# Kernel optimization log

Measured on AMD Instinct MI355X. Metric: run time of the kernel, lower is better.

The kernel has to match this reference:

```python
import jax, jax.numpy as jnp
import numpy as np

LN_EPS = 1e-5

def _layernorm(x, w, b):
    mu = jnp.mean(x, axis=-1, keepdims=True)
    var = jnp.mean(jnp.square(x - mu), axis=-1, keepdims=True)
    return (x - mu) * jax.lax.rsqrt(var + LN_EPS) * w + b

def setup_inputs() -> dict:
    key = jax.random.key(0)
    ks = jax.random.split(key, 6)
    B, NQ, QD = 8, 576, 4096
    NKV, KVD = 2304, 1024
    s = 0.02
    return {
        "x_q": jax.random.normal(ks[0], (B, NQ, QD), jnp.float32),
        "x_kv": jax.random.normal(ks[1], (B, NKV, KVD), jnp.float32),
        "q_ln_w": jnp.ones((QD,), jnp.float32),
        "q_ln_b": jnp.zeros((QD,), jnp.float32),
        "q_w": jax.random.normal(ks[2], (QD, QD), jnp.float32) * s,
        "q_b": jnp.zeros((QD,), jnp.float32),
        "k_ln_w": jnp.ones((KVD,), jnp.float32),
        "k_ln_b": jnp.zeros((KVD,), jnp.float32),
        "k_w": jax.random.normal(ks[3], (KVD, QD), jnp.float32) * s,
        "k_b": jnp.zeros((QD,), jnp.float32),
        "v_ln_w": jnp.ones((KVD,), jnp.float32),
        "v_ln_b": jnp.zeros((KVD,), jnp.float32),
        "v_w": jax.random.normal(ks[4], (KVD, QD), jnp.float32) * s,
        "v_b": jnp.zeros((QD,), jnp.float32),
    }

def reference(x_q, x_kv, q_ln_w, q_ln_b, q_w, q_b,
              k_ln_w, k_ln_b, k_w, k_b, v_ln_w, v_ln_b, v_w, v_b):
    B, NQ, QD = x_q.shape
    hw = int(round(x_kv.shape[1] ** 0.5))          # 48
    KVD = x_kv.shape[-1]
    patch_num = int(round(NQ ** 0.5))              # 24
    patch_size = hw // patch_num                   # 2
    # 'b (h w) d -> b h w d' then group into patch_num x patch_num windows
    kv = x_kv.reshape(B, hw, hw, KVD)
    kv = kv.reshape(B, patch_num, patch_size, patch_num, patch_size, KVD)
    kv = kv.transpose(0, 1, 3, 2, 4, 5).reshape(B, patch_num * patch_num, patch_size * patch_size, KVD)
    # projections (LayerNorm + Linear)
    q = _layernorm(x_q, q_ln_w, q_ln_b) @ q_w + q_b            # [B, P2, QD]
    k = _layernorm(kv, k_ln_w, k_ln_b) @ k_w + k_b             # [B, P2, S2, QD]
    v = _layernorm(kv, v_ln_w, v_ln_b) @ v_w + v_b             # [B, P2, S2, QD]
    scale = 1.0 / (QD ** 0.5)
    att = jnp.einsum('bpd,bpsd->bps', q, k) * scale            # [B, P2, S2]
    att = jnp.nan_to_num(att)
    att = jax.nn.softmax(att, axis=-1)
    feat = jnp.einsum('bps,bpsd->bpd', att, v)                 # [B, P2, QD]
    return (x_q, feat)
```

## Files before the change

kernel.cpp:

```cpp
#include <hip/hip_runtime.h>
#include <cstdint>
#include <cstddef>


typedef __attribute__((ext_vector_type(8))) short short8;
typedef __attribute__((ext_vector_type(4))) float f32x4;

#define DEV __device__ __forceinline__

DEV unsigned short f2bf(float f) {
  union { float f; unsigned u; } x; x.f = f;
  unsigned r = x.u + 0x7fffu + ((x.u >> 16) & 1u);
  return (unsigned short)(r >> 16);
}
DEV float bf2f(unsigned short u) {
  union { unsigned u; float f; } x; x.u = ((unsigned)u) << 16;
  return x.f;
}

DEV void gload16(const void* g, void* l) {
  __builtin_amdgcn_global_load_lds(
      (const __attribute__((address_space(1))) unsigned int*)g,
      (__attribute__((address_space(3))) unsigned int*)l, 16, 0, 0);
}

template <bool OUT_BF16, bool HAS_BIAS>
__global__ __launch_bounds__(256, 2) void gemm_nt(
    const unsigned short* __restrict__ A, const unsigned short* __restrict__ Bm,
    void* __restrict__ Cv, const float* __restrict__ bias, int M, int N, int K) {
  __shared__ __align__(16) unsigned short lds_a[128 * 32];
  __shared__ __align__(16) unsigned short lds_b[128 * 32];
  const int t = threadIdx.x;
  const int l = t & 63;
  const int w = t >> 6;
  const long brow = (long)blockIdx.x * 128;
  const long bcol = (long)blockIdx.y * 128;

  const int srow = t >> 2;
  const int scol = (t & 3) * 8;
  const unsigned short* a0 = A + (brow + srow) * (long)K + scol;
  const unsigned short* a1 = A + (brow + 64 + srow) * (long)K + scol;
  const unsigned short* b0 = Bm + (bcol + srow) * (long)K + scol;
  const unsigned short* b1 = Bm + (bcol + 64 + srow) * (long)K + scol;
  unsigned short* la0 = lds_a + t * 8;
  unsigned short* la1 = lds_a + 2048 + t * 8;
  unsigned short* lb0 = lds_b + t * 8;
  unsigned short* lb1 = lds_b + 2048 + t * 8;

  const int wr = w >> 1, wc = w & 1;
  const int fr = l & 15;
  const int fk = (l >> 4) * 8;

  f32x4 acc[4][4] = {};

  for (int kt = 0; kt < K; kt += 32) {
    __syncthreads();
    gload16(a0 + kt, la0);
    gload16(a1 + kt, la1);
    gload16(b0 + kt, lb0);
    gload16(b1 + kt, lb1);
    asm volatile("s_waitcnt vmcnt(0)" ::: "memory");
    __syncthreads();
    short8 af[4], bf[4];
#pragma unroll
    for (int mi = 0; mi < 4; ++mi)
      af[mi] = *(const short8*)&lds_a[(wr * 64 + mi * 16 + fr) * 32 + fk];
#pragma unroll
    for (int ni = 0; ni < 4; ++ni)
      bf[ni] = *(const short8*)&lds_b[(wc * 64 + ni * 16 + fr) * 32 + fk];
#pragma unroll
    for (int mi = 0; mi < 4; ++mi)
#pragma unroll
      for (int ni = 0; ni < 4; ++ni)
        acc[mi][ni] = __builtin_amdgcn_mfma_f32_16x16x32_bf16(af[mi], bf[ni],
                                                              acc[mi][ni], 0, 0, 0);
  }

  const int crow = (l >> 4) * 4;
#pragma unroll
  for (int ni = 0; ni < 4; ++ni) {
    const long col = bcol + wc * 64 + ni * 16 + fr;
    const float bv = HAS_BIAS ? bias[col] : 0.0f;
#pragma unroll
    for (int mi = 0; mi < 4; ++mi) {
#pragma unroll
      for (int r = 0; r < 4; ++r) {
        const long row = brow + wr * 64 + mi * 16 + crow + r;
        const float v = acc[mi][ni][r] + bv;
        if (OUT_BF16)
          ((unsigned short*)Cv)[row * (long)N + col] = f2bf(v);
        else
          ((float*)Cv)[row * (long)N + col] = v;
      }
    }
  }
}

__global__ __launch_bounds__(256) void ln_q_kernel(
    const float* __restrict__ x, const float* __restrict__ w,
    const float* __restrict__ b, float* __restrict__ copy_out,
    unsigned short* __restrict__ qn) {
  const int row = blockIdx.x, t = threadIdx.x;
  const float4* xr = (const float4*)(x + (size_t)row * 4096);
  float4 v[4];
  float s = 0.f, s2 = 0.f;
#pragma unroll
  for (int j = 0; j < 4; ++j) {
    v[j] = xr[j * 256 + t];
    s += v[j].x + v[j].y + v[j].z + v[j].w;
    s2 += v[j].x * v[j].x + v[j].y * v[j].y + v[j].z * v[j].z + v[j].w * v[j].w;
  }
#pragma unroll
  for (int off = 32; off; off >>= 1) {
    s += __shfl_xor(s, off);
    s2 += __shfl_xor(s2, off);
  }
  __shared__ float red[8];
  if ((t & 63) == 0) { red[t >> 6] = s; red[4 + (t >> 6)] = s2; }
  __syncthreads();
  s = red[0] + red[1] + red[2] + red[3];
  s2 = red[4] + red[5] + red[6] + red[7];
  const float mu = s * (1.f / 4096.f);
  const float rstd = rsqrtf(s2 * (1.f / 4096.f) - mu * mu + 1e-5f);
  float4* co = (float4*)(copy_out + (size_t)row * 4096);
  unsigned short* qr = qn + (size_t)row * 4096;
#pragma unroll
  for (int j = 0; j < 4; ++j) {
    co[j * 256 + t] = v[j];
    const int c = (j * 256 + t) * 4;
    const float4 wv = *(const float4*)(w + c);
    const float4 bv = *(const float4*)(b + c);
    ushort4 o = make_ushort4(f2bf((v[j].x - mu) * rstd * wv.x + bv.x),
                             f2bf((v[j].y - mu) * rstd * wv.y + bv.y),
                             f2bf((v[j].z - mu) * rstd * wv.z + bv.z),
                             f2bf((v[j].w - mu) * rstd * wv.w + bv.w));
    *(ushort4*)(qr + c) = o;
  }
}

__global__ __launch_bounds__(256) void ln_kv_kernel(
    const float* __restrict__ x, const float* __restrict__ kw,
    const float* __restrict__ kb, const float* __restrict__ vw,
    const float* __restrict__ vb, unsigned short* __restrict__ kn,
    unsigned short* __restrict__ vn) {
  const int row = blockIdx.x, t = threadIdx.x;
  const float4 v = ((const float4*)(x + (size_t)row * 1024))[t];
  float s = v.x + v.y + v.z + v.w;
  float s2 = v.x * v.x + v.y * v.y + v.z * v.z + v.w * v.w;
#pragma unroll
  for (int off = 32; off; off >>= 1) {
    s += __shfl_xor(s, off);
    s2 += __shfl_xor(s2, off);
  }
  __shared__ float red[8];
  if ((t & 63) == 0) { red[t >> 6] = s; red[4 + (t >> 6)] = s2; }
  __syncthreads();
  s = red[0] + red[1] + red[2] + red[3];
  s2 = red[4] + red[5] + red[6] + red[7];
  const float mu = s * (1.f / 1024.f);
  const float rstd = rsqrtf(s2 * (1.f / 1024.f) - mu * mu + 1e-5f);
  const int c = t * 4;
  const float4 kw4 = *(const float4*)(kw + c);
  const float4 kb4 = *(const float4*)(kb + c);
  const float4 vw4 = *(const float4*)(vw + c);
  const float4 vb4 = *(const float4*)(vb + c);
  const float h0 = (v.x - mu) * rstd, h1 = (v.y - mu) * rstd;
  const float h2 = (v.z - mu) * rstd, h3 = (v.w - mu) * rstd;
  *(ushort4*)(kn + (size_t)row * 1024 + c) =
      make_ushort4(f2bf(h0 * kw4.x + kb4.x), f2bf(h1 * kw4.y + kb4.y),
                   f2bf(h2 * kw4.z + kb4.z), f2bf(h3 * kw4.w + kb4.w));
  *(ushort4*)(vn + (size_t)row * 1024 + c) =
      make_ushort4(f2bf(h0 * vw4.x + vb4.x), f2bf(h1 * vw4.y + vb4.y),
                   f2bf(h2 * vw4.z + vb4.z), f2bf(h3 * vw4.w + vb4.w));
}

__global__ __launch_bounds__(256) void conv_bf16(
    const float* __restrict__ src, unsigned short* __restrict__ dst, int n4) {
  int i = blockIdx.x * 256 + threadIdx.x;
  const int stride = gridDim.x * 256;
  for (; i < n4; i += stride) {
    const float4 v = ((const float4*)src)[i];
    ((ushort4*)dst)[i] = make_ushort4(f2bf(v.x), f2bf(v.y), f2bf(v.z), f2bf(v.w));
  }
}

__global__ void transpose_conv(const float* __restrict__ src,
                               unsigned short* __restrict__ dst) {
  __shared__ float tile[32][33];
  const int n0 = blockIdx.x * 32, k0 = blockIdx.y * 32;
  const int tx = threadIdx.x, ty = threadIdx.y;
#pragma unroll
  for (int i = 0; i < 32; i += 8)
    tile[ty + i][tx] = src[(size_t)(k0 + ty + i) * 4096 + n0 + tx];
  __syncthreads();
#pragma unroll
  for (int i = 0; i < 32; i += 8)
    dst[(size_t)(n0 + ty + i) * 1024 + k0 + tx] = f2bf(tile[tx][ty + i]);
}

__global__ __launch_bounds__(256) void qkb_kernel(const float* __restrict__ qb,
                                                  const float* __restrict__ kw,
                                                  float* __restrict__ out) {
  const int c = blockIdx.x, t = threadIdx.x;
  const float4* kr = (const float4*)(kw + (size_t)c * 4096);
  const float4* q4 = (const float4*)qb;
  float s = 0.f;
#pragma unroll
  for (int j = 0; j < 4; ++j) {
    const float4 a = q4[j * 256 + t], b = kr[j * 256 + t];
    s += a.x * b.x + a.y * b.y + a.z * b.z + a.w * b.w;
  }
#pragma unroll
  for (int off = 32; off; off >>= 1) s += __shfl_xor(s, off);
  __shared__ float red[4];
  if ((t & 63) == 0) red[t >> 6] = s;
  __syncthreads();
  if (t == 0) out[c] = red[0] + red[1] + red[2] + red[3];
}

__global__ __launch_bounds__(256) void att_kernel(
    const float* __restrict__ qk, const unsigned short* __restrict__ kn,
    const unsigned short* __restrict__ vn, unsigned short* __restrict__ wkv) {
  const int m = blockIdx.x;
  const int b = m / 576, p = m % 576;
  const int py = p / 24, px = p % 24;
  const int t = threadIdx.x, w = t >> 6, l = t & 63;

  const size_t row_w =
      (size_t)b * 2304 + (size_t)(py * 2 + (w >> 1)) * 48 + (px * 2 + (w & 1));
  const float* qrow = qk + (size_t)m * 1024;
  const unsigned short* krow = kn + row_w * 1024;
  float dot = 0.f;
#pragma unroll
  for (int j = 0; j < 4; ++j) {
    const int c = j * 256 + l * 4;
    const float4 q4 = *(const float4*)(qrow + c);
    const ushort4 k4 = *(const ushort4*)(krow + c);
    dot += q4.x * bf2f(k4.x) + q4.y * bf2f(k4.y) + q4.z * bf2f(k4.z) +
           q4.w * bf2f(k4.w);
  }
#pragma unroll
  for (int off = 32; off; off >>= 1) dot += __shfl_xor(dot, off);
  __shared__ float lg[4];
  if (l == 0) lg[w] = dot * 0.015625f;
  __syncthreads();
  const float l0 = lg[0], l1 = lg[1], l2 = lg[2], l3 = lg[3];
  const float mx = fmaxf(fmaxf(l0, l1), fmaxf(l2, l3));
  float e0 = __expf(l0 - mx), e1 = __expf(l1 - mx);
  float e2 = __expf(l2 - mx), e3 = __expf(l3 - mx);
  const float inv = 1.f / (e0 + e1 + e2 + e3);
  const float at[4] = {e0 * inv, e1 * inv, e2 * inv, e3 * inv};

  const int c = t * 4;
  float a0 = 0.f, a1 = 0.f, a2 = 0.f, a3 = 0.f;
#pragma unroll
  for (int s = 0; s < 4; ++s) {
    const size_t row_s =
        (size_t)b * 2304 + (size_t)(py * 2 + (s >> 1)) * 48 + (px * 2 + (s & 1));
    const ushort4 v4 = *(const ushort4*)(vn + row_s * 1024 + c);
    a0 += at[s] * bf2f(v4.x);
    a1 += at[s] * bf2f(v4.y);
    a2 += at[s] * bf2f(v4.z);
    a3 += at[s] * bf2f(v4.w);
  }
  *(ushort4*)(wkv + (size_t)m * 1024 + c) =
      make_ushort4(f2bf(a0), f2bf(a1), f2bf(a2), f2bf(a3));
}

extern "C" void kernel_launch(void* const* d_in, const int* in_sizes, int n_in,
                              void* d_out, int out_size, void* d_ws,
                              size_t ws_size, hipStream_t stream) {
  const float* x_q = (const float*)d_in[0];
  const float* x_kv = (const float*)d_in[1];
  const float* q_ln_w = (const float*)d_in[2];
  const float* q_ln_b = (const float*)d_in[3];
  const float* q_w = (const float*)d_in[4];
  const float* q_b = (const float*)d_in[5];
  const float* k_ln_w = (const float*)d_in[6];
  const float* k_ln_b = (const float*)d_in[7];
  const float* k_w = (const float*)d_in[8];
  const float* v_ln_w = (const float*)d_in[10];
  const float* v_ln_b = (const float*)d_in[11];
  const float* v_w = (const float*)d_in[12];
  const float* v_b = (const float*)d_in[13];

  char* ws = (char*)d_ws;
  unsigned short* qn = (unsigned short*)(ws);
  unsigned short* kn = (unsigned short*)(ws + 37748736);
  unsigned short* vn = (unsigned short*)(ws + 75497472);
  unsigned short* qwb = (unsigned short*)(ws + 113246208);
  unsigned short* kwb = (unsigned short*)(ws + 146800640);
  unsigned short* Wt = (unsigned short*)(ws + 155189248);
  unsigned short* vwT = (unsigned short*)(ws + 163577856);
  float* qk = (float*)(ws + 171966464);
  float* qkbv = (float*)(ws + 190840832);
  unsigned short* wkv = (unsigned short*)(ws + 190844928);

  float* out0 = (float*)d_out;
  float* out1 = out0 + (size_t)4608 * 4096;

  ln_q_kernel<<<4608, 256, 0, stream>>>(x_q, q_ln_w, q_ln_b, out0, qn);
  ln_kv_kernel<<<18432, 256, 0, stream>>>(x_kv, k_ln_w, k_ln_b, v_ln_w, v_ln_b,
                                          kn, vn);
  conv_bf16<<<4096, 256, 0, stream>>>(q_w, qwb, 4096 * 4096 / 4);
  conv_bf16<<<1024, 256, 0, stream>>>(k_w, kwb, 1024 * 4096 / 4);
  transpose_conv<<<dim3(128, 32), dim3(32, 8), 0, stream>>>(v_w, vwT);
  qkb_kernel<<<1024, 256, 0, stream>>>(q_b, k_w, qkbv);
  gemm_nt<true, false><<<dim3(8, 32), 256, 0, stream>>>(kwb, qwb, Wt, nullptr,
                                                        1024, 4096, 4096);
  gemm_nt<false, true><<<dim3(36, 8), 256, 0, stream>>>(qn, Wt, qk, qkbv, 4608,
                                                        1024, 4096);
  att_kernel<<<4608, 256, 0, stream>>>(qk, kn, vn, wkv);
  gemm_nt<false, true><<<dim3(36, 32), 256, 0, stream>>>(wkv, vwT, out1, v_b,
                                                         4608, 4096, 1024);
}
```

Baseline: 622.7 us.

## Add split-K with reduction kernel and XCD-aware block remapping to GEMMs

Adds a split-K mode to the NT GEMM: the two K=4096 GEMMs (weight fold and q×W) launch with a z-dimension of up to 4 K-chunks, each writing fp32 partials that a new reduce kernel sums, then adds bias and converts to bf16 or fp32. This raises block count for the grids of 256 and 288 blocks so more CUs stay busy. Block indices are also remapped in groups of 8, presumably to spread neighbouring tiles across XCDs. The trade-off is extra partial-sum traffic to global memory and two additional kernel launches.

```diff
diff --git a/kernel.cpp b/kernel.cpp
--- a/kernel.cpp
+++ b/kernel.cpp
@@ -24,24 +24,37 @@
       (__attribute__((address_space(3))) unsigned int*)l, 16, 0, 0);
 }
 
-template <bool OUT_BF16, bool HAS_BIAS>
+template <bool PARTIAL, bool OUT_BF16, bool HAS_BIAS>
 __global__ __launch_bounds__(256, 2) void gemm_nt(
     const unsigned short* __restrict__ A, const unsigned short* __restrict__ Bm,
-    void* __restrict__ Cv, const float* __restrict__ bias, int M, int N, int K) {
+    void* __restrict__ Cv, const float* __restrict__ bias, int M, int N,
+    int Kfull, int Kchunk) {
   __shared__ __align__(16) unsigned short lds_a[128 * 32];
   __shared__ __align__(16) unsigned short lds_b[128 * 32];
   const int t = threadIdx.x;
   const int l = t & 63;
   const int w = t >> 6;
-  const long brow = (long)blockIdx.x * 128;
-  const long bcol = (long)blockIdx.y * 128;
+
+  int bx = blockIdx.x, by = blockIdx.y;
+  {
+    const int nbx = gridDim.x, nby = gridDim.y;
+    const int nwg = nbx * nby;
+    int flat = by * nbx + bx;
+    flat = (flat & 7) * (nwg >> 3) + (flat >> 3);
+    bx = flat % nbx;
+    by = flat / nbx;
+  }
+  const long brow = (long)bx * 128;
+  const long bcol = (long)by * 128;
+  const int z = blockIdx.z;
+  const int k0 = z * Kchunk;
 
   const int srow = t >> 2;
   const int scol = (t & 3) * 8;
-  const unsigned short* a0 = A + (brow + srow) * (long)K + scol;
-  const unsigned short* a1 = A + (brow + 64 + srow) * (long)K + scol;
-  const unsigned short* b0 = Bm + (bcol + srow) * (long)K + scol;
-  const unsigned short* b1 = Bm + (bcol + 64 + srow) * (long)K + scol;
+  const unsigned short* a0 = A + (brow + srow) * (long)Kfull + scol + k0;
+  const unsigned short* a1 = A + (brow + 64 + srow) * (long)Kfull + scol + k0;
+  const unsigned short* b0 = Bm + (bcol + srow) * (long)Kfull + scol + k0;
+  const unsigned short* b1 = Bm + (bcol + 64 + srow) * (long)Kfull + scol + k0;
   unsigned short* la0 = lds_a + t * 8;
   unsigned short* la1 = lds_a + 2048 + t * 8;
   unsigned short* lb0 = lds_b + t * 8;
@@ -53,7 +66,7 @@
 
   f32x4 acc[4][4] = {};
 
-  for (int kt = 0; kt < K; kt += 32) {
+  for (int kt = 0; kt < Kchunk; kt += 32) {
     __syncthreads();
     gload16(a0 + kt, la0);
     gload16(a1 + kt, la1);
@@ -61,38 +74,67 @@
     gload16(b1 + kt, lb1);
     asm volatile("s_waitcnt vmcnt(0)" ::: "memory");
     __syncthreads();
-    short8 af[4], bf[4];
+    short8 af[4], bfr[4];
 #pragma unroll
     for (int mi = 0; mi < 4; ++mi)
       af[mi] = *(const short8*)&lds_a[(wr * 64 + mi * 16 + fr) * 32 + fk];
 #pragma unroll
     for (int ni = 0; ni < 4; ++ni)
-      bf[ni] = *(const short8*)&lds_b[(wc * 64 + ni * 16 + fr) * 32 + fk];
+      bfr[ni] = *(const short8*)&lds_b[(wc * 64 + ni * 16 + fr) * 32 + fk];
 #pragma unroll
     for (int mi = 0; mi < 4; ++mi)
 #pragma unroll
       for (int ni = 0; ni < 4; ++ni)
-        acc[mi][ni] = __builtin_amdgcn_mfma_f32_16x16x32_bf16(af[mi], bf[ni],
+        acc[mi][ni] = __builtin_amdgcn_mfma_f32_16x16x32_bf16(af[mi], bfr[ni],
                                                               acc[mi][ni], 0, 0, 0);
   }
 
   const int crow = (l >> 4) * 4;
+  float* Cpart = PARTIAL ? ((float*)Cv + (size_t)z * M * (size_t)N) : nullptr;
 #pragma unroll
   for (int ni = 0; ni < 4; ++ni) {
     const long col = bcol + wc * 64 + ni * 16 + fr;
-    const float bv = HAS_BIAS ? bias[col] : 0.0f;
+    const float bv = (!PARTIAL && HAS_BIAS) ? bias[col] : 0.0f;
 #pragma unroll
     for (int mi = 0; mi < 4; ++mi) {
 #pragma unroll
       for (int r = 0; r < 4; ++r) {
         const long row = brow + wr * 64 + mi * 16 + crow + r;
         const float v = acc[mi][ni][r] + bv;
-        if (OUT_BF16)
+        if (PARTIAL)
+          Cpart[row * (long)N + col] = v;
+        else if (OUT_BF16)
           ((unsigned short*)Cv)[row * (long)N + col] = f2bf(v);
         else
           ((float*)Cv)[row * (long)N + col] = v;
       }
     }
+  }
+}
+
+template <bool OUT_BF16, bool HAS_BIAS>
+__global__ __launch_bounds__(256) void reduce_splits(
+    const float* __restrict__ part, void* __restrict__ out,
+    const float* __restrict__ bias, int S, size_t MN, int nmask) {
+  size_t i = (size_t)blockIdx.x * 256 + threadIdx.x;
+  const size_t n4 = MN / 4;
+  const size_t stride = (size_t)gridDim.x * 256;
+  for (; i < n4; i += stride) {
+    float4 a = ((const float4*)part)[i];
+    for (int s = 1; s < S; ++s) {
+      const float4 b = ((const float4*)(part + (size_t)s * MN))[i];
+      a.x += b.x; a.y += b.y; a.z += b.z; a.w += b.w;
+    }
+    if (HAS_BIAS) {
+      const int c = (int)((i * 4) & (size_t)nmask);
+      const float4 bv = *(const float4*)(bias + c);
+      a.x += bv.x; a.y += bv.y; a.z += bv.z; a.w += bv.w;
+    }
+    if (OUT_BF16)
+      ((ushort4*)out)[i] =
+          make_ushort4(f2bf(a.x), f2bf(a.y), f2bf(a.z), f2bf(a.w));
+    else
+      ((float4*)out)[i] = a;
   }
 }
 
@@ -295,6 +337,14 @@
   float* qk = (float*)(ws + 171966464);
   float* qkbv = (float*)(ws + 190840832);
   unsigned short* wkv = (unsigned short*)(ws + 190844928);
+  float* part = (float*)(ws + 200282112);
+
+  const size_t MN_W = (size_t)1024 * 4096;
+  const size_t MN_QK = (size_t)4608 * 1024;
+  int splitW = 1, splitQK = 1;
+  if (ws_size >= 200282112 + 4 * MN_QK * 4) { splitW = 4; splitQK = 4; }
+  else if (ws_size >= 200282112 + 2 * MN_QK * 4) { splitW = 2; splitQK = 2; }
+  const bool partial_ok = ws_size >= 200282112 + MN_QK * 4;
 
   float* out0 = (float*)d_out;
   float* out1 = out0 + (size_t)4608 * 4096;
@@ -306,11 +356,24 @@
   conv_bf16<<<1024, 256, 0, stream>>>(k_w, kwb, 1024 * 4096 / 4);
   transpose_conv<<<dim3(128, 32), dim3(32, 8), 0, stream>>>(v_w, vwT);
   qkb_kernel<<<1024, 256, 0, stream>>>(q_b, k_w, qkbv);
-  gemm_nt<true, false><<<dim3(8, 32), 256, 0, stream>>>(kwb, qwb, Wt, nullptr,
-                                                        1024, 4096, 4096);
-  gemm_nt<false, true><<<dim3(36, 8), 256, 0, stream>>>(qn, Wt, qk, qkbv, 4608,
-                                                        1024, 4096);
+
+  if (partial_ok) {
+    gemm_nt<true, false, false><<<dim3(8, 32, splitW), 256, 0, stream>>>(
+        kwb, qwb, part, nullptr, 1024, 4096, 4096, 4096 / splitW);
+    reduce_splits<true, false><<<2048, 256, 0, stream>>>(part, Wt, nullptr,
+                                                         splitW, MN_W, 0);
+    gemm_nt<true, false, false><<<dim3(36, 8, splitQK), 256, 0, stream>>>(
+        qn, Wt, part, nullptr, 4608, 1024, 4096, 4096 / splitQK);
+    reduce_splits<false, true><<<2048, 256, 0, stream>>>(part, qk, qkbv,
+                                                         splitQK, MN_QK, 1023);
+  } else {
+    gemm_nt<false, true, false><<<dim3(8, 32), 256, 0, stream>>>(
+        kwb, qwb, Wt, nullptr, 1024, 4096, 4096, 4096);
+    gemm_nt<false, false, true><<<dim3(36, 8), 256, 0, stream>>>(
+        qn, Wt, qk, qkbv, 4608, 1024, 4096, 4096);
+  }
+
   att_kernel<<<4608, 256, 0, stream>>>(qk, kn, vn, wkv);
-  gemm_nt<false, true><<<dim3(36, 32), 256, 0, stream>>>(wkv, vwT, out1, v_b,
-                                                         4608, 4096, 1024);
-}
+  gemm_nt<false, false, true><<<dim3(36, 32), 256, 0, stream>>>(
+      wkv, vwT, out1, v_b, 4608, 4096, 1024, 1024);
+}
```

New measurement: 603.8 us. 1.03x faster.
